# Optimization experiments

Measured on AMD Instinct MI355X. Metric: run time of the kernel, lower is better.

Reference implementation:

```python
import jax, jax.numpy as jnp
import numpy as np

T, B, C, H = 1024, 4, 1024, 16
NH = C // H  # head_size = 64
E = 32       # TIME_MIX_EXTRA_DIM


def setup_inputs():
    key = jax.random.key(0)
    ks = jax.random.split(key, 12)
    scale = 1.0 / np.sqrt(C)

    def time_p(ratio):
        w = jnp.arange(C, dtype=jnp.float32) / C
        return (1.0 - jnp.power(w, ratio))[None, None, :]

    decay_speed = jnp.array([-6.0 + 5.0 * (h / (C - 1)) ** 0.7 for h in range(C)], jnp.float32)
    tfa = jnp.array([0.1 * ((i + 1) % 3 - 1) for i in range(C)], jnp.float32).reshape(H, NH)
    return dict(
        inputs=jax.random.normal(ks[0], (T, B, C), jnp.float32),
        shifted=jax.random.normal(ks[1], (B, C), jnp.float32),
        state=jnp.zeros((B, H, NH, NH), jnp.float32),
        time_maa_x=time_p(1.0), time_maa_w=time_p(1.0), time_maa_k=time_p(1.0),
        time_maa_v=time_p(1.0), time_maa_r=time_p(0.5), time_maa_g=time_p(0.5),
        time_maa_w1=jax.random.uniform(ks[2], (C, E * 5), jnp.float32, -1e-4, 1e-4),
        time_maa_w2=jax.random.uniform(ks[3], (5, E, C), jnp.float32, -1e-4, 1e-4),
        Wr=jax.random.normal(ks[4], (C, C), jnp.float32) * scale,
        Wk=jax.random.normal(ks[5], (C, C), jnp.float32) * scale,
        Wv=jax.random.normal(ks[6], (C, C), jnp.float32) * scale,
        Wg=jax.random.normal(ks[7], (C, C), jnp.float32) * scale,
        Wo=jax.random.normal(ks[8], (C, C), jnp.float32) * scale,
        time_decay_w1=jax.random.uniform(ks[9], (C, E), jnp.float32, -1e-4, 1e-4),
        time_decay_w2=jax.random.uniform(ks[10], (E, C), jnp.float32, -1e-4, 1e-4),
        time_decay=decay_speed[None, None, :],
        time_faaaa=tfa,
        gn_scale=jnp.ones((C,), jnp.float32) + 0.02 * jax.random.normal(ks[11], (C,), jnp.float32),
        gn_bias=jnp.zeros((C,), jnp.float32),
    )


def _wkv(r, k, v, w, tf, state):
    # r,k,v,w: (T,B,H,N); tf: (H,N,1); state: (B,H,N,N)
    def body(st, inp):
        rt, kt, vt, wt = inp
        a = kt[..., :, None] * vt[..., None, :]              # (B,H,N,N) outer product
        out = jnp.einsum('bhn,bhnm->bhm', rt, tf * a + st)   # (B,H,N)
        st = a + wt[..., None] * st
        return st, out
    state, out = jax.lax.scan(body, state, (r, k, v, w))
    return out, state


def reference(inputs, shifted, state, time_maa_x, time_maa_w, time_maa_k,
              time_maa_v, time_maa_r, time_maa_g, time_maa_w1, time_maa_w2,
              Wr, Wk, Wv, Wg, Wo, time_decay_w1, time_decay_w2, time_decay,
              time_faaaa, gn_scale, gn_bias):
    Tl, Bl, Cl = inputs.shape
    Hh, Nh = time_faaaa.shape
    x = inputs
    prev = jnp.concatenate([shifted[None], inputs[:-1]], axis=0)  # token shift
    xx = prev - x
    new_shifted = inputs[-1]
    xxx = x + xx * time_maa_x
    m = jnp.tanh(xxx.reshape(Tl * Bl, Cl) @ time_maa_w1).reshape(Tl * Bl, 5, -1).transpose(1, 0, 2)
    m = (m @ time_maa_w2).reshape(5, Tl, Bl, Cl)
    mw, mk, mv, mr, mg = m[0], m[1], m[2], m[3], m[4]
    r = (x + xx * (time_maa_r + mr)) @ Wr
    k = (x + xx * (time_maa_k + mk)) @ Wk
    v = (x + xx * (time_maa_v + mv)) @ Wv
    g = jax.nn.swish((x + xx * (time_maa_g + mg)) @ Wg)
    td = jnp.tanh((x + xx * (time_maa_w + mw)) @ time_decay_w1) @ time_decay_w2 + time_decay
    w = jnp.exp(-jnp.exp(td)).reshape(Tl, Bl, Hh, Nh)
    out, new_state = _wkv(r.reshape(Tl, Bl, Hh, Nh), k.reshape(Tl, Bl, Hh, Nh),
                          v.reshape(Tl, Bl, Hh, Nh), w, time_faaaa[:, :, None], state)
    # flax GroupNorm with leading axis as batch: stats over (B, within-group chans)
    xg = out.reshape(Tl, Bl, Hh, Nh)
    mean = xg.mean(axis=(1, 3), keepdims=True)
    var = xg.var(axis=(1, 3), keepdims=True)
    xn = (xg - mean) * jax.lax.rsqrt(var + 1e-5 * 8.0 ** 2)
    out = xn.reshape(Tl, Bl, Cl) * gn_scale + gn_bias
    out = (out * g) @ Wo
    return out, new_shifted, new_state
```

## Files before the change

### kernel.cpp

```cpp
#include <hip/hip_runtime.h>

using uint = unsigned int;
using ushort = unsigned short;
using f32x4 = __attribute__((ext_vector_type(4))) float;
using bf16x8 = __attribute__((ext_vector_type(8))) short;

__device__ __forceinline__ ushort f2bf(float x) {
  uint b = __float_as_uint(x);
  return (ushort)((b + 0x7FFFu + ((b >> 16) & 1u)) >> 16);
}
__device__ __forceinline__ float bf2f(ushort u) { return __uint_as_float(((uint)u) << 16); }

__device__ __forceinline__ void gload16(const void* g, void* l) {
  __builtin_amdgcn_global_load_lds((const __attribute__((address_space(1))) void*)g,
                                   (__attribute__((address_space(3))) void*)l, 16, 0, 0);
}
__device__ __forceinline__ void gload4(const void* g, void* l) {
  __builtin_amdgcn_global_load_lds((const __attribute__((address_space(1))) void*)g,
                                   (__attribute__((address_space(3))) void*)l, 4, 0, 0);
}

struct __align__(8) U4 { ushort x, y, z, w; };

__device__ __forceinline__ void convT_impl(const float* src, ushort* oh, ushort* ol, int R, int C, int ldo) {
  const int r0 = blockIdx.x * 32, c0 = blockIdx.y * 32;
  if (r0 >= ldo || c0 >= C) return;
  __shared__ float tile[32][33];
  const int tx = threadIdx.x & 31, ty = threadIdx.x >> 5;
#pragma unroll
  for (int j = 0; j < 4; ++j) {
    const int r = r0 + ty + j * 8;
    tile[ty + j * 8][tx] = (r < R) ? src[(size_t)r * C + c0 + tx] : 0.f;
  }
  __syncthreads();
#pragma unroll
  for (int j = 0; j < 4; ++j) {
    const int c = c0 + ty + j * 8;
    const int r = r0 + tx;
    const float v = tile[tx][ty + j * 8];
    const ushort hb = f2bf(v);
    oh[(size_t)c * ldo + r] = hb;
    if (ol) ol[(size_t)c * ldo + r] = f2bf(v - bf2f(hb));
  }
}

struct ConvBig { const float* s[5]; ushort* oh[5]; ushort* ol[5]; };
__global__ void conv_big_k(ConvBig a) {
  const int z = blockIdx.z;
  convT_impl(a.s[z], a.oh[z], a.ol[z], 1024, 1024, 1024);
}

struct ConvSmall { const float* s[8]; ushort* oh[8]; int R[8]; int C[8]; int ldo[8]; };
__global__ void conv_small_k(ConvSmall a) {
  const int z = blockIdx.z;
  convT_impl(a.s[z], a.oh[z], nullptr, a.R[z], a.C[z], a.ldo[z]);
}

__global__ void mixx_k(const float* __restrict__ x, const float* __restrict__ sh,
                       const float* __restrict__ maa, ushort* __restrict__ xh) {
  const size_t i = ((size_t)blockIdx.x * 256 + threadIdx.x) * 4;
  const size_t row = i >> 10;
  const int col = (int)(i & 1023);
  const float4 xv = *(const float4*)(x + i);
  const float4 pv = (row < 4) ? *(const float4*)(sh + i) : *(const float4*)(x + i - 4096);
  const float4 mv = *(const float4*)(maa + col);
  U4 o;
  o.x = f2bf(xv.x + (pv.x - xv.x) * mv.x);
  o.y = f2bf(xv.y + (pv.y - xv.y) * mv.y);
  o.z = f2bf(xv.z + (pv.z - xv.z) * mv.z);
  o.w = f2bf(xv.w + (pv.w - xv.w) * mv.w);
  *(U4*)(xh + i) = o;
}

struct GemmP {
  const ushort *Ah, *Al, *Bh, *Bl;
  void *out0, *out1;
  const float *aux0, *aux1, *aux2;
  int lda, ldb, M, N, K, epi, split;
};

__device__ __forceinline__ bf16x8 fragld(const ushort* smbase, int byteOff, int rb, int ks, int l) {
  const int row = rb + (l & 15);
  const int kb = (ks << 6) | (((l >> 4) & 3) << 4);
  const int off = byteOff + row * 128 + (kb ^ ((row & 7) << 4));
  return *(const bf16x8*)((const char*)smbase + off);
}

__global__ __launch_bounds__(256, 2) void gemm_k(GemmP p) {
  __shared__ __align__(16) ushort sm[32768];
  const int t = threadIdx.x;
  const int l = t & 63, wid = t >> 6;
  const int wm = wid >> 1, wn = wid & 1;
  const int bm = blockIdx.x, bn = blockIdx.y;

  f32x4 acc[4][4];
#pragma unroll
  for (int i = 0; i < 4; ++i)
#pragma unroll
    for (int j = 0; j < 4; ++j) acc[i][j] = (f32x4){0.f, 0.f, 0.f, 0.f};

  const int srow = t >> 3;
  const int skb = (t & 7) << 4;
  const int KT = (p.K + 63) >> 6;

  for (int kt = 0; kt < KT; ++kt) {
    const int k0 = kt << 6;
    __syncthreads();
#pragma unroll
    for (int j = 0; j < 4; ++j) {
      const int row = srow + j * 32;
      const int srcK = k0 + ((skb ^ ((row & 7) << 4)) >> 1);
      gload16(p.Ah + (size_t)(bm * 128 + row) * p.lda + srcK, (char*)sm + row * 128 + skb);
      gload16(p.Bh + (size_t)(bn * 128 + row) * p.ldb + srcK, (char*)sm + 16384 + row * 128 + skb);
    }
    if (p.split) {
#pragma unroll
      for (int j = 0; j < 4; ++j) {
        const int row = srow + j * 32;
        const int srcK = k0 + ((skb ^ ((row & 7) << 4)) >> 1);
        gload16(p.Al + (size_t)(bm * 128 + row) * p.lda + srcK, (char*)sm + 32768 + row * 128 + skb);
        gload16(p.Bl + (size_t)(bn * 128 + row) * p.ldb + srcK, (char*)sm + 49152 + row * 128 + skb);
      }
    }
    __syncthreads();
#pragma unroll
    for (int ks = 0; ks < 2; ++ks) {
      bf16x8 ah[4], bh[4];
#pragma unroll
      for (int f = 0; f < 4; ++f) {
        ah[f] = fragld(sm, 0, wm * 64 + f * 16, ks, l);
        bh[f] = fragld(sm, 16384, wn * 64 + f * 16, ks, l);
      }
      if (p.split) {
        bf16x8 al[4], bl[4];
#pragma unroll
        for (int f = 0; f < 4; ++f) {
          al[f] = fragld(sm, 32768, wm * 64 + f * 16, ks, l);
          bl[f] = fragld(sm, 49152, wn * 64 + f * 16, ks, l);
        }
#pragma unroll
        for (int mf = 0; mf < 4; ++mf)
#pragma unroll
          for (int nf = 0; nf < 4; ++nf) {
            acc[mf][nf] = __builtin_amdgcn_mfma_f32_16x16x32_bf16(ah[mf], bh[nf], acc[mf][nf], 0, 0, 0);
            acc[mf][nf] = __builtin_amdgcn_mfma_f32_16x16x32_bf16(ah[mf], bl[nf], acc[mf][nf], 0, 0, 0);
            acc[mf][nf] = __builtin_amdgcn_mfma_f32_16x16x32_bf16(al[mf], bh[nf], acc[mf][nf], 0, 0, 0);
          }
      } else {
#pragma unroll
        for (int mf = 0; mf < 4; ++mf)
#pragma unroll
          for (int nf = 0; nf < 4; ++nf)
            acc[mf][nf] = __builtin_amdgcn_mfma_f32_16x16x32_bf16(ah[mf], bh[nf], acc[mf][nf], 0, 0, 0);
      }
    }
  }

  const int rb0 = bm * 128 + wm * 64 + ((l >> 4) << 2);
  const int cb0 = bn * 128 + wn * 64 + (l & 15);
#pragma unroll
  for (int mf = 0; mf < 4; ++mf) {
#pragma unroll
    for (int nf = 0; nf < 4; ++nf) {
      const int col = cb0 + nf * 16;
      if (col >= p.N) continue;
#pragma unroll
      for (int jj = 0; jj < 4; ++jj) {
        const int row = rb0 + mf * 16 + jj;
        const float v = acc[mf][nf][jj];
        const size_t o = (size_t)row * p.N + col;
        if (p.epi == 0) {
          ((float*)p.out0)[o] = v;
        } else if (p.epi == 1) {
          ((ushort*)p.out0)[o] = f2bf(tanhf(v));
        } else if (p.epi == 2) {
          ((float*)p.out0)[o] = v / (1.f + expf(-v));
        } else if (p.epi == 3) {
          const float x = p.aux0[(size_t)row * 1024 + col];
          const float pv = (row < 4) ? p.aux1[(size_t)row * 1024 + col]
                                     : p.aux0[(size_t)(row - 4) * 1024 + col];
          const float xi = x + (pv - x) * (p.aux2[col] + v);
          const ushort hb = f2bf(xi);
          ((ushort*)p.out0)[o] = hb;
          ((ushort*)p.out1)[o] = f2bf(xi - bf2f(hb));
        } else {
          ((float*)p.out0)[o] = expf(-expf(v + p.aux0[col]));
        }
      }
    }
  }
}

__global__ __launch_bounds__(256) void wkv_k(const float* __restrict__ rf, const float* __restrict__ kf,
                                             const float* __restrict__ vf, const float* __restrict__ wf,
                                             const float* __restrict__ tf, const float* __restrict__ st0,
                                             float* __restrict__ so, float* __restrict__ stO) {
  __shared__ __align__(16) float sr[2][32][64], sk[2][32][64], sw[2][32][64];
  __shared__ __align__(16) float sv[2][32][8];
  const int tl = threadIdx.x;
  const int l = tl & 63, wid = tl >> 6;
  const int bh = blockIdx.x & 63;
  const int mg = blockIdx.x >> 6;
  const int b = bh >> 4, h = bh & 15;
  const int ml = wid * 2 + (l >> 5);
  const int m = mg * 8 + ml;
  const int n = (l & 31) << 1;
  const size_t bOff = (size_t)b * 1024 + h * 64;

  const size_t sOff = ((size_t)bh * 64 + n) * 64 + m;
  float s0 = st0[sOff], s1 = st0[sOff + 64];
  const float u0 = tf[h * 64 + n], u1 = tf[h * 64 + n + 1];

  const int tloc = tl >> 4;
  const int n4 = (tl & 15) << 2;
  const int tv = tl >> 3, mv = tl & 7;

  auto stage = [&](int bufS, int c) {
    const size_t g0 = (size_t)(c << 5) * 4096 + bOff;
    const size_t ga = g0 + (size_t)tloc * 4096 + n4;
    gload16(rf + ga, &sr[bufS][tloc][n4]);
    gload16(kf + ga, &sk[bufS][tloc][n4]);
    gload16(wf + ga, &sw[bufS][tloc][n4]);
    const size_t gb = ga + 16 * 4096;
    gload16(rf + gb, &sr[bufS][tloc + 16][n4]);
    gload16(kf + gb, &sk[bufS][tloc + 16][n4]);
    gload16(wf + gb, &sw[bufS][tloc + 16][n4]);
    gload4(vf + g0 + (size_t)tv * 4096 + (mg << 3) + mv, &sv[bufS][tv][mv]);
  };

  stage(0, 0);
  size_t obase = bOff;
  int buf = 0;
  for (int c = 0; c < 32; ++c) {
    __syncthreads();
    if (c + 1 < 32) stage(buf ^ 1, c + 1);
#pragma unroll 4
    for (int tt = 0; tt < 32; ++tt) {
      const float2 r2 = *(const float2*)&sr[buf][tt][n];
      const float2 k2 = *(const float2*)&sk[buf][tt][n];
      const float2 w2 = *(const float2*)&sw[buf][tt][n];
      const float vm = sv[buf][tt][ml];
      const float kv0 = k2.x * vm, kv1 = k2.y * vm;
      float pr = r2.x * fmaf(u0, kv0, s0) + r2.y * fmaf(u1, kv1, s1);
      s0 = fmaf(w2.x, s0, kv0);
      s1 = fmaf(w2.y, s1, kv1);
      pr += __shfl_xor(pr, 1);
      pr += __shfl_xor(pr, 2);
      pr += __shfl_xor(pr, 4);
      pr += __shfl_xor(pr, 8);
      pr += __shfl_xor(pr, 16);
      if ((l & 31) == 0) so[obase + m] = pr;
      obase += 4096;
    }
    buf ^= 1;
  }
  stO[sOff] = s0;
  stO[sOff + 64] = s1;
}

__global__ __launch_bounds__(256) void gn_k(const float* __restrict__ so, const float* __restrict__ gf,
                                            const float* __restrict__ sc, const float* __restrict__ bi,
                                            ushort* __restrict__ yh, ushort* __restrict__ yl) {
  const int tdx = threadIdx.x;
  const int b = tdx >> 6, n = tdx & 63;
  const int t = blockIdx.x, h = blockIdx.y;
  const size_t idx = (size_t)t * 4096 + (size_t)b * 1024 + h * 64 + n;
  const float v = so[idx];
  float s = v, s2 = v * v;
#pragma unroll
  for (int off = 1; off < 64; off <<= 1) {
    s += __shfl_xor(s, off);
    s2 += __shfl_xor(s2, off);
  }
  __shared__ float ps[4], ps2[4];
  if ((tdx & 63) == 0) { ps[b] = s; ps2[b] = s2; }
  __syncthreads();
  const float S = ps[0] + ps[1] + ps[2] + ps[3];
  const float S2 = ps2[0] + ps2[1] + ps2[2] + ps2[3];
  const float mean = S * (1.f / 256.f);
  const float var = S2 * (1.f / 256.f) - mean * mean;
  const float inv = rsqrtf(var + 6.4e-4f);
  const int c = h * 64 + n;
  float y = (v - mean) * inv * sc[c] + bi[c];
  y *= gf[idx];
  const ushort hb = f2bf(y);
  yh[idx] = hb;
  yl[idx] = f2bf(y - bf2f(hb));
}

extern "C" void kernel_launch(void* const* d_in, const int* in_sizes, int n_in,
                              void* d_out, int out_size, void* d_ws, size_t ws_size,
                              hipStream_t stream) {
  const float* inp = (const float*)d_in[0];
  const float* shifted = (const float*)d_in[1];
  const float* st0 = (const float*)d_in[2];
  const float* maa_x = (const float*)d_in[3];
  const float* maa[5] = {(const float*)d_in[4], (const float*)d_in[5], (const float*)d_in[6],
                         (const float*)d_in[7], (const float*)d_in[8]};
  const float* w1 = (const float*)d_in[9];
  const float* w2 = (const float*)d_in[10];
  const float* W[5] = {(const float*)d_in[11], (const float*)d_in[12], (const float*)d_in[13],
                       (const float*)d_in[14], (const float*)d_in[15]};
  const float* tdw1 = (const float*)d_in[16];
  const float* tdw2 = (const float*)d_in[17];
  const float* tdec = (const float*)d_in[18];
  const float* tf = (const float*)d_in[19];
  const float* gsc = (const float*)d_in[20];
  const float* gbi = (const float*)d_in[21];
  (void)in_sizes; (void)n_in; (void)out_size; (void)ws_size;

  char* ws = (char*)d_ws;
  size_t cur = 0;
  auto alloc = [&](size_t bytes) { char* r = ws + cur; cur += (bytes + 255) & ~(size_t)255; return r; };
  ushort *WT_h[5], *WT_l[5];
  for (int i = 0; i < 5; ++i) {
    WT_h[i] = (ushort*)alloc(1024 * 1024 * 2);
    WT_l[i] = (ushort*)alloc(1024 * 1024 * 2);
  }
  ushort* w1T = (ushort*)alloc(256 * 1024 * 2);
  ushort* tdw1T = (ushort*)alloc(128 * 1024 * 2);
  ushort* tdw2T = (ushort*)alloc(1024 * 64 * 2);
  ushort* w2T = (ushort*)alloc(5 * 1024 * 64 * 2);
  ushort* xxh = (ushort*)alloc(4096ull * 1024 * 2);
  ushort* m1h = (ushort*)alloc(4096ull * 160 * 2 + 256);
  ushort* Xh = (ushort*)alloc(4096ull * 1024 * 2);
  ushort* Xl = (ushort*)alloc(4096ull * 1024 * 2);
  ushort* tdhh = (ushort*)alloc(4096ull * 32 * 2 + 256);
  float* r_f = (float*)alloc(16777216);
  float* k_f = (float*)alloc(16777216);
  float* v_f = (float*)alloc(16777216);
  float* w_f = (float*)alloc(16777216);
  float* g_f = (float*)alloc(16777216);
  float* so_f = (float*)alloc(16777216);
  ushort* yh = (ushort*)alloc(8388608);
  ushort* yl = (ushort*)alloc(8388608);

  ConvBig cb;
  for (int i = 0; i < 5; ++i) { cb.s[i] = W[i]; cb.oh[i] = WT_h[i]; cb.ol[i] = WT_l[i]; }
  conv_big_k<<<dim3(32, 32, 5), 256, 0, stream>>>(cb);
  ConvSmall cs;
  cs.s[0] = w1;   cs.oh[0] = w1T;   cs.R[0] = 1024; cs.C[0] = 160;  cs.ldo[0] = 1024;
  cs.s[1] = tdw1; cs.oh[1] = tdw1T; cs.R[1] = 1024; cs.C[1] = 32;   cs.ldo[1] = 1024;
  cs.s[2] = tdw2; cs.oh[2] = tdw2T; cs.R[2] = 32;   cs.C[2] = 1024; cs.ldo[2] = 64;
  for (int i = 0; i < 5; ++i) {
    cs.s[3 + i] = w2 + (size_t)i * 32 * 1024;
    cs.oh[3 + i] = w2T + (size_t)i * 1024 * 64;
    cs.R[3 + i] = 32; cs.C[3 + i] = 1024; cs.ldo[3 + i] = 64;
  }
  conv_small_k<<<dim3(32, 32, 8), 256, 0, stream>>>(cs);

  mixx_k<<<dim3(4096), 256, 0, stream>>>(inp, shifted, maa_x, xxh);

  auto G = [&](const ushort* Ah, const ushort* Al, int lda, const ushort* Bh, const ushort* Bl, int ldb,
               int N, int K, void* out0, void* out1, int epi, int split,
               const float* a0, const float* a1, const float* a2) {
    GemmP p{Ah, Al, Bh, Bl, out0, out1, a0, a1, a2, lda, ldb, 4096, N, K, epi, split};
    gemm_k<<<dim3(32, (N + 127) / 128), 256, 0, stream>>>(p);
  };

  G(xxh, nullptr, 1024, w1T, nullptr, 1024, 160, 1024, m1h, nullptr, 1, 0, nullptr, nullptr, nullptr);
  G(m1h + 0, nullptr, 160, w2T + 0 * 65536, nullptr, 64, 1024, 32, Xh, Xl, 3, 0, inp, shifted, maa[0]);
  G(Xh, nullptr, 1024, tdw1T, nullptr, 1024, 32, 1024, tdhh, nullptr, 1, 0, nullptr, nullptr, nullptr);
  G(m1h + 96, nullptr, 160, w2T + 3 * 65536, nullptr, 64, 1024, 32, Xh, Xl, 3, 0, inp, shifted, maa[3]);
  G(Xh, Xl, 1024, WT_h[0], WT_l[0], 1024, 1024, 1024, r_f, nullptr, 0, 1, nullptr, nullptr, nullptr);
  G(m1h + 32, nullptr, 160, w2T + 1 * 65536, nullptr, 64, 1024, 32, Xh, Xl, 3, 0, inp, shifted, maa[1]);
  G(Xh, Xl, 1024, WT_h[1], WT_l[1], 1024, 1024, 1024, k_f, nullptr, 0, 1, nullptr, nullptr, nullptr);
  G(m1h + 64, nullptr, 160, w2T + 2 * 65536, nullptr, 64, 1024, 32, Xh, Xl, 3, 0, inp, shifted, maa[2]);
  G(Xh, Xl, 1024, WT_h[2], WT_l[2], 1024, 1024, 1024, v_f, nullptr, 0, 1, nullptr, nullptr, nullptr);
  G(m1h + 128, nullptr, 160, w2T + 4 * 65536, nullptr, 64, 1024, 32, Xh, Xl, 3, 0, inp, shifted, maa[4]);
  G(Xh, Xl, 1024, WT_h[3], WT_l[3], 1024, 1024, 1024, g_f, nullptr, 2, 1, nullptr, nullptr, nullptr);
  G(tdhh, nullptr, 32, tdw2T, nullptr, 64, 1024, 32, w_f, nullptr, 4, 0, tdec, nullptr, nullptr);

  float* stateOut = (float*)d_out + 4194304 + 4096;
  wkv_k<<<dim3(512), 256, 0, stream>>>(r_f, k_f, v_f, w_f, tf, st0, so_f, stateOut);
  gn_k<<<dim3(1024, 16), 256, 0, stream>>>(so_f, g_f, gsc, gbi, yh, yl);
  G(yh, yl, 1024, WT_h[4], WT_l[4], 1024, 1024, 1024, (float*)d_out, nullptr, 0, 1, nullptr, nullptr, nullptr);
  hipMemcpyAsync((float*)d_out + 4194304, inp + 4096ull * 1023, 4096 * sizeof(float),
                 hipMemcpyDeviceToDevice, stream);
}
```

Measured before the change: 883.2 us.

## Give each WKV thread eight state columns and halve block count

The WKV recurrence kernel is remapped so each thread holds eight state entries along n instead of two. That shrinks the per-timestep shuffle reduction from five steps to three and lets the kernel read r, k and w with float4 LDS loads. Blocks shrink to 128 threads and the grid to 256 blocks, each covering 16 output columns, and v staging uses 16-byte loads. The aim is less reduction and shuffle overhead per timestep, at the cost of fewer resident waves on the sequential critical path.

```diff
diff --git a/kernel.cpp b/kernel.cpp
--- a/kernel.cpp
+++ b/kernel.cpp
@@ -14,10 +14,6 @@
 __device__ __forceinline__ void gload16(const void* g, void* l) {
   __builtin_amdgcn_global_load_lds((const __attribute__((address_space(1))) void*)g,
                                    (__attribute__((address_space(3))) void*)l, 16, 0, 0);
-}
-__device__ __forceinline__ void gload4(const void* g, void* l) {
-  __builtin_amdgcn_global_load_lds((const __attribute__((address_space(1))) void*)g,
-                                   (__attribute__((address_space(3))) void*)l, 4, 0, 0);
 }
 
 struct __align__(8) U4 { ushort x, y, z, w; };
@@ -191,71 +187,89 @@
   }
 }
 
-__global__ __launch_bounds__(256) void wkv_k(const float* __restrict__ rf, const float* __restrict__ kf,
+#define TCH 32
+__global__ __launch_bounds__(128) void wkv_k(const float* __restrict__ rf, const float* __restrict__ kf,
                                              const float* __restrict__ vf, const float* __restrict__ wf,
                                              const float* __restrict__ tf, const float* __restrict__ st0,
                                              float* __restrict__ so, float* __restrict__ stO) {
-  __shared__ __align__(16) float sr[2][32][64], sk[2][32][64], sw[2][32][64];
-  __shared__ __align__(16) float sv[2][32][8];
+  __shared__ __align__(16) float sr[2][TCH][64], sk[2][TCH][64], sw[2][TCH][64], sv[2][TCH][16];
   const int tl = threadIdx.x;
   const int l = tl & 63, wid = tl >> 6;
   const int bh = blockIdx.x & 63;
   const int mg = blockIdx.x >> 6;
   const int b = bh >> 4, h = bh & 15;
-  const int ml = wid * 2 + (l >> 5);
-  const int m = mg * 8 + ml;
-  const int n = (l & 31) << 1;
+  const int slice = l & 7;
+  const int ml = (wid << 3) + (l >> 3);
+  const int m = (mg << 4) + ml;
+  const int n0 = slice << 3;
   const size_t bOff = (size_t)b * 1024 + h * 64;
 
-  const size_t sOff = ((size_t)bh * 64 + n) * 64 + m;
-  float s0 = st0[sOff], s1 = st0[sOff + 64];
-  const float u0 = tf[h * 64 + n], u1 = tf[h * 64 + n + 1];
-
-  const int tloc = tl >> 4;
-  const int n4 = (tl & 15) << 2;
-  const int tv = tl >> 3, mv = tl & 7;
+  float s[8], u[8];
+  const size_t sBase = ((size_t)bh * 64 + n0) * 64 + m;
+#pragma unroll
+  for (int j = 0; j < 8; ++j) s[j] = st0[sBase + (size_t)j * 64];
+#pragma unroll
+  for (int j = 0; j < 8; ++j) u[j] = tf[h * 64 + n0 + j];
+
+  const int tq = tl >> 4;
+  const int c16 = (tl & 15) << 2;
+  const int tv = tl >> 2, jv = (tl & 3) << 2;
 
   auto stage = [&](int bufS, int c) {
-    const size_t g0 = (size_t)(c << 5) * 4096 + bOff;
-    const size_t ga = g0 + (size_t)tloc * 4096 + n4;
-    gload16(rf + ga, &sr[bufS][tloc][n4]);
-    gload16(kf + ga, &sk[bufS][tloc][n4]);
-    gload16(wf + ga, &sw[bufS][tloc][n4]);
-    const size_t gb = ga + 16 * 4096;
-    gload16(rf + gb, &sr[bufS][tloc + 16][n4]);
-    gload16(kf + gb, &sk[bufS][tloc + 16][n4]);
-    gload16(wf + gb, &sw[bufS][tloc + 16][n4]);
-    gload4(vf + g0 + (size_t)tv * 4096 + (mg << 3) + mv, &sv[bufS][tv][mv]);
+    const size_t g0 = (size_t)(c * TCH) * 4096 + bOff;
+#pragma unroll
+    for (int q = 0; q < 4; ++q) {
+      const int trow = q * 8 + tq;
+      const size_t ga = g0 + (size_t)trow * 4096 + c16;
+      gload16(rf + ga, &sr[bufS][trow][c16]);
+      gload16(kf + ga, &sk[bufS][trow][c16]);
+      gload16(wf + ga, &sw[bufS][trow][c16]);
+    }
+    gload16(vf + g0 + (size_t)tv * 4096 + (mg << 4) + jv, &sv[bufS][tv][jv]);
   };
 
   stage(0, 0);
-  size_t obase = bOff;
   int buf = 0;
-  for (int c = 0; c < 32; ++c) {
+  for (int c = 0; c < 1024 / TCH; ++c) {
     __syncthreads();
-    if (c + 1 < 32) stage(buf ^ 1, c + 1);
+    if (c + 1 < 1024 / TCH) stage(buf ^ 1, c + 1);
 #pragma unroll 4
-    for (int tt = 0; tt < 32; ++tt) {
-      const float2 r2 = *(const float2*)&sr[buf][tt][n];
-      const float2 k2 = *(const float2*)&sk[buf][tt][n];
-      const float2 w2 = *(const float2*)&sw[buf][tt][n];
-      const float vm = sv[buf][tt][ml];
-      const float kv0 = k2.x * vm, kv1 = k2.y * vm;
-      float pr = r2.x * fmaf(u0, kv0, s0) + r2.y * fmaf(u1, kv1, s1);
-      s0 = fmaf(w2.x, s0, kv0);
-      s1 = fmaf(w2.y, s1, kv1);
+    for (int t = 0; t < TCH; ++t) {
+      const float4 ra = *(const float4*)&sr[buf][t][n0];
+      const float4 rb = *(const float4*)&sr[buf][t][n0 + 4];
+      const float4 ka = *(const float4*)&sk[buf][t][n0];
+      const float4 kb = *(const float4*)&sk[buf][t][n0 + 4];
+      const float4 wa = *(const float4*)&sw[buf][t][n0];
+      const float4 wb = *(const float4*)&sw[buf][t][n0 + 4];
+      const float vm = sv[buf][t][ml];
+      const float kv0 = ka.x * vm, kv1 = ka.y * vm, kv2 = ka.z * vm, kv3 = ka.w * vm;
+      const float kv4 = kb.x * vm, kv5 = kb.y * vm, kv6 = kb.z * vm, kv7 = kb.w * vm;
+      float pA = ra.x * fmaf(u[0], kv0, s[0]);
+      pA = fmaf(ra.y, fmaf(u[1], kv1, s[1]), pA);
+      float pB = ra.z * fmaf(u[2], kv2, s[2]);
+      pB = fmaf(ra.w, fmaf(u[3], kv3, s[3]), pB);
+      float pC = rb.x * fmaf(u[4], kv4, s[4]);
+      pC = fmaf(rb.y, fmaf(u[5], kv5, s[5]), pC);
+      float pD = rb.z * fmaf(u[6], kv6, s[6]);
+      pD = fmaf(rb.w, fmaf(u[7], kv7, s[7]), pD);
+      s[0] = fmaf(wa.x, s[0], kv0);
+      s[1] = fmaf(wa.y, s[1], kv1);
+      s[2] = fmaf(wa.z, s[2], kv2);
+      s[3] = fmaf(wa.w, s[3], kv3);
+      s[4] = fmaf(wb.x, s[4], kv4);
+      s[5] = fmaf(wb.y, s[5], kv5);
+      s[6] = fmaf(wb.z, s[6], kv6);
+      s[7] = fmaf(wb.w, s[7], kv7);
+      float pr = (pA + pB) + (pC + pD);
       pr += __shfl_xor(pr, 1);
       pr += __shfl_xor(pr, 2);
       pr += __shfl_xor(pr, 4);
-      pr += __shfl_xor(pr, 8);
-      pr += __shfl_xor(pr, 16);
-      if ((l & 31) == 0) so[obase + m] = pr;
-      obase += 4096;
+      if (slice == 0) so[(size_t)(c * TCH + t) * 4096 + bOff + m] = pr;
     }
     buf ^= 1;
   }
-  stO[sOff] = s0;
-  stO[sOff + 64] = s1;
+#pragma unroll
+  for (int j = 0; j < 8; ++j) stO[sBase + (size_t)j * 64] = s[j];
 }
 
 __global__ __launch_bounds__(256) void gn_k(const float* __restrict__ so, const float* __restrict__ gf,
@@ -372,7 +386,7 @@
   G(tdhh, nullptr, 32, tdw2T, nullptr, 64, 1024, 32, w_f, nullptr, 4, 0, tdec, nullptr, nullptr);
 
   float* stateOut = (float*)d_out + 4194304 + 4096;
-  wkv_k<<<dim3(512), 256, 0, stream>>>(r_f, k_f, v_f, w_f, tf, st0, so_f, stateOut);
+  wkv_k<<<dim3(256), 128, 0, stream>>>(r_f, k_f, v_f, w_f, tf, st0, so_f, stateOut);
   gn_k<<<dim3(1024, 16), 256, 0, stream>>>(so_f, g_f, gsc, gbi, yh, yl);
   G(yh, yl, 1024, WT_h[4], WT_l[4], 1024, 1024, 1024, (float*)d_out, nullptr, 0, 1, nullptr, nullptr, nullptr);
   hipMemcpyAsync((float*)d_out + 4194304, inp + 4096ull * 1023, 4096 * sizeof(float),
```

New measurement: 869.2 us. About the same (-1.6%).
